# Performance work log

Hardware: AMD Instinct MI355X
Metric: run time of the kernel (lower is better)

## Reference

```python
import jax, jax.numpy as jnp
import numpy as np

E, NB, F, H = 30, 12, 1024, 32  # numEmotions, numBasicEmotions, numCommonFeatures, hidden
EPS = 1e-12  # F.normalize eps


def setup_inputs() -> dict:
    key = jax.random.key(0)
    ks = jax.random.split(key, 7)
    B, L = 8192, 128
    return {
        "basicEmotionDistributions": jax.random.uniform(ks[0], (B, NB, L), dtype=jnp.float32),
        "encodedFeatures": jax.random.normal(ks[1], (B, F), dtype=jnp.float32),
        "allBasicEmotionWeights": jax.random.normal(ks[2], (E, 1, NB, 1), dtype=jnp.float32),
        "W1": jax.random.normal(ks[3], (E, F, H), dtype=jnp.float32) / np.sqrt(F),
        "b1": jax.random.normal(ks[4], (E, H), dtype=jnp.float32) * 0.01,
        "W2": jax.random.normal(ks[5], (E, H, NB), dtype=jnp.float32) / np.sqrt(H),
        "b2": jax.random.normal(ks[6], (E, NB), dtype=jnp.float32) * 0.01,
    }


def reference(basicEmotionDistributions, encodedFeatures, allBasicEmotionWeights, W1, b1, W2, b2):
    # L1-normalize exp(weights) along basic-emotion dim: (E, NB)
    ew = jnp.exp(allBasicEmotionWeights[:, 0, :, 0])  # (E, NB)
    allW = ew / jnp.maximum(jnp.sum(jnp.abs(ew), axis=1, keepdims=True), EPS)

    # Batched per-emotion 2-layer MLP: (E, B, NB)
    h = jax.nn.selu(jnp.einsum('bf,efh->ebh', encodedFeatures, W1) + b1[:, None, :])
    mlp = jnp.einsum('ebh,ehn->ebn', h, W2) + b2[:, None, :]

    # updated weights and signed L1 normalization over NB dim
    updated = allW[:, None, :] + mlp  # (E, B, NB)
    # sign(x) * normalize(|x|, p=1) == x / max(sum|x|, eps)
    w = updated / jnp.maximum(jnp.sum(jnp.abs(updated), axis=2, keepdims=True), EPS)

    # weighted sum over basic emotions, then softmax over emotion length
    mixed = jnp.einsum('ebn,bnl->ebl', w, basicEmotionDistributions)  # (E, B, L)
    return jax.nn.softmax(mixed, axis=2)
```

## Files before the change

### kernel.cpp

```cpp
#include <hip/hip_runtime.h>

#define E_ 30
#define NB_ 12
#define F_ 1024
#define H_ 32
#define B_ 8192
#define L_ 128

typedef __attribute__((ext_vector_type(8))) _Float16 half8;
typedef __attribute__((ext_vector_type(4))) float f32x4;

#define GAS(p) ((const __attribute__((address_space(1))) void*)(p))
#define LAS(p) ((__attribute__((address_space(3))) void*)(p))

__global__ __launch_bounds__(256) void cvtA(const float* __restrict__ feat,
                                            _Float16* __restrict__ out) {
    int gid = blockIdx.x * 256 + threadIdx.x;
    int k8   = gid & 3;
    int m    = (gid >> 2) & 15;
    int frag = gid >> 6;
    int mf = frag & 7;
    int kc = (frag >> 3) & 31;
    int bt = frag >> 8;
    int b  = bt * 128 + mf * 16 + m;
    int f0 = kc * 32 + k8 * 8;
    const float4* src = (const float4*)(feat + (size_t)b * 1024 + f0);
    float4 v0 = src[0], v1 = src[1];
    half8 o;
    o[0] = (_Float16)v0.x; o[1] = (_Float16)v0.y;
    o[2] = (_Float16)v0.z; o[3] = (_Float16)v0.w;
    o[4] = (_Float16)v1.x; o[5] = (_Float16)v1.y;
    o[6] = (_Float16)v1.z; o[7] = (_Float16)v1.w;
    *(half8*)(out + ((size_t)frag * 64 + k8 * 16 + m) * 8) = o;
}

__global__ __launch_bounds__(256) void cvtW1(const float* __restrict__ W1,
                                             _Float16* __restrict__ out) {
    int gid = blockIdx.x * 256 + threadIdx.x;
    int k8   = gid & 3;
    int n    = (gid >> 2) & 15;
    int frag = gid >> 6;
    int nf = frag & 1;
    int kc = (frag >> 1) & 31;
    int e  = frag >> 6;
    int h  = nf * 16 + n;
    int f0 = kc * 32 + k8 * 8;
    const float* src = W1 + ((size_t)e * 1024 + f0) * 32 + h;
    half8 o;
#pragma unroll
    for (int j = 0; j < 8; ++j) o[j] = (_Float16)src[j * 32];
    *(half8*)(out + ((size_t)frag * 64 + k8 * 16 + n) * 8) = o;
}

__global__ __launch_bounds__(256) void gemm_mlp(
    const _Float16* __restrict__ A16, const _Float16* __restrict__ W1T,
    const float* __restrict__ b1, const float* __restrict__ W2,
    const float* __restrict__ b2, const float* __restrict__ wts,
    float* __restrict__ wbuf) {
    __shared__ __align__(16) unsigned char smem[22400];
    float* h_sh = (float*)smem;
    unsigned char* Ash = smem;
    unsigned char* Bsh = smem + 16384;
    float* w2s = (float*)(smem + 20480);
    float* cb2 = (float*)(smem + 20480 + 1536);
    float* ews = cb2 + 12;

    const int tid = threadIdx.x;
    const int e  = blockIdx.x;
    const int bt = blockIdx.y;
    const int w  = tid >> 6, l = tid & 63;
    const int q  = l >> 4, lc = l & 15;

    for (int i = tid; i < 384; i += 256) w2s[i] = W2[e * 384 + i];
    if (tid < 12) {
        cb2[tid] = b2[e * 12 + tid];
        ews[tid] = __expf(wts[e * 12 + tid]);
    }

    const _Float16* Abase = A16 + (size_t)bt * 131072;
    const _Float16* Bbase = W1T + (size_t)e * 32768;

    f32x4 zero = {0.f, 0.f, 0.f, 0.f};
    f32x4 acc[2][2];
    acc[0][0] = zero; acc[0][1] = zero; acc[1][0] = zero; acc[1][1] = zero;

    for (int it = 0; it < 16; ++it) {
        const _Float16* Ait = Abase + it * 8192;
        const _Float16* Bit = Bbase + it * 2048;
#pragma unroll
        for (int i = 0; i < 4; ++i) {
            int s = w * 4 + i;
            __builtin_amdgcn_global_load_lds(GAS(Ait + s * 512 + l * 8),
                                             LAS(Ash + s * 1024), 16, 0, 0);
        }
        __builtin_amdgcn_global_load_lds(GAS(Bit + w * 512 + l * 8),
                                         LAS(Bsh + w * 1024), 16, 0, 0);
        __syncthreads();
#pragma unroll
        for (int kc2 = 0; kc2 < 2; ++kc2) {
            half8 a0  = *(half8*)(Ash + (kc2 * 8 + 2 * w + 0) * 1024 + l * 16);
            half8 a1  = *(half8*)(Ash + (kc2 * 8 + 2 * w + 1) * 1024 + l * 16);
            half8 bv0 = *(half8*)(Bsh + (kc2 * 2 + 0) * 1024 + l * 16);
            half8 bv1 = *(half8*)(Bsh + (kc2 * 2 + 1) * 1024 + l * 16);
            acc[0][0] = __builtin_amdgcn_mfma_f32_16x16x32_f16(a0, bv0, acc[0][0], 0, 0, 0);
            acc[0][1] = __builtin_amdgcn_mfma_f32_16x16x32_f16(a0, bv1, acc[0][1], 0, 0, 0);
            acc[1][0] = __builtin_amdgcn_mfma_f32_16x16x32_f16(a1, bv0, acc[1][0], 0, 0, 0);
            acc[1][1] = __builtin_amdgcn_mfma_f32_16x16x32_f16(a1, bv1, acc[1][1], 0, 0, 0);
        }
        __syncthreads();
    }

    const float b1v0 = b1[e * 32 + lc];
    const float b1v1 = b1[e * 32 + 16 + lc];
    const float SC = 1.0507009873554805f, AL = 1.6732632423543772f;
#pragma unroll
    for (int mf = 0; mf < 2; ++mf)
#pragma unroll
        for (int nf = 0; nf < 2; ++nf)
#pragma unroll
            for (int r = 0; r < 4; ++r) {
                int m   = w * 32 + mf * 16 + q * 4 + r;
                int col = nf * 16 + lc;
                float x = acc[mf][nf][r] + (nf ? b1v1 : b1v0);
                float hv = x > 0.f ? SC * x : SC * AL * (__expf(x) - 1.f);
                h_sh[m * 33 + col] = hv;
            }
    __syncthreads();

    const int m2 = tid >> 1, sub = tid & 1;
    float u[6] = {0.f, 0.f, 0.f, 0.f, 0.f, 0.f};
    const float* hrow = h_sh + m2 * 33;
#pragma unroll 8
    for (int h = 0; h < 32; ++h) {
        float hv = hrow[h];
        const float* wr = w2s + h * 12 + sub * 6;
#pragma unroll
        for (int j = 0; j < 6; ++j) u[j] += hv * wr[j];
    }
    float sew = 0.f;
#pragma unroll
    for (int i = 0; i < 12; ++i) sew += ews[i];
    sew = fmaxf(sew, 1e-12f);
    float sabs = 0.f;
#pragma unroll
    for (int j = 0; j < 6; ++j) {
        u[j] += cb2[sub * 6 + j] + ews[sub * 6 + j] / sew;
        sabs += fabsf(u[j]);
    }
    sabs += __shfl_xor(sabs, 1);
    float inv = 1.f / fmaxf(sabs, 1e-12f);
    int b = bt * 128 + m2;
    float* dst = wbuf + (size_t)b * 360 + e * 12 + sub * 6;
#pragma unroll
    for (int j = 0; j < 6; ++j) dst[j] = u[j] * inv;
}

__global__ __launch_bounds__(256) void mix_softmax(
    const float* __restrict__ dist, const float* __restrict__ wbuf,
    float* __restrict__ out) {
    __shared__ float wsm[8 * 360];
    const int tid = threadIdx.x;
    const int b0 = blockIdx.x * 8;
    for (int i = tid; i < 2880; i += 256) wsm[i] = wbuf[(size_t)b0 * 360 + i];
    __syncthreads();
    const int m = tid >> 5, l4 = tid & 31;
    const int b = b0 + m;
    const float* dbase = dist + (size_t)b * 1536 + l4 * 4;
    f32x4 d[12];
#pragma unroll
    for (int n = 0; n < 12; ++n) d[n] = *(const f32x4*)(dbase + n * 128);
    const float* wrow = wsm + m * 360;
    for (int e = 0; e < 30; ++e) {
        const float* wr = wrow + e * 12;
        f32x4 a = {0.f, 0.f, 0.f, 0.f};
#pragma unroll
        for (int n = 0; n < 12; ++n) a += wr[n] * d[n];
        float mx = fmaxf(fmaxf(a[0], a[1]), fmaxf(a[2], a[3]));
#pragma unroll
        for (int s = 16; s >= 1; s >>= 1) mx = fmaxf(mx, __shfl_xor(mx, s));
        f32x4 ex;
        ex[0] = __expf(a[0] - mx); ex[1] = __expf(a[1] - mx);
        ex[2] = __expf(a[2] - mx); ex[3] = __expf(a[3] - mx);
        float sm = ex[0] + ex[1] + ex[2] + ex[3];
#pragma unroll
        for (int s = 16; s >= 1; s >>= 1) sm += __shfl_xor(sm, s);
        f32x4 o = ex * (1.f / sm);
        *(f32x4*)(out + ((size_t)e * 8192 + b) * 128 + l4 * 4) = o;
    }
}

extern "C" void kernel_launch(void* const* d_in, const int* in_sizes, int n_in,
                              void* d_out, int out_size, void* d_ws, size_t ws_size,
                              hipStream_t stream) {
    const float* dist = (const float*)d_in[0];
    const float* feat = (const float*)d_in[1];
    const float* wts  = (const float*)d_in[2];
    const float* W1   = (const float*)d_in[3];
    const float* b1   = (const float*)d_in[4];
    const float* W2   = (const float*)d_in[5];
    const float* b2   = (const float*)d_in[6];
    float* out = (float*)d_out;

    _Float16* A16 = (_Float16*)d_ws;
    _Float16* W1T = (_Float16*)((char*)d_ws + 16777216);
    float*   wbuf = (float*)((char*)d_ws + 16777216 + 1966080);

    cvtA<<<4096, 256, 0, stream>>>(feat, A16);
    cvtW1<<<480, 256, 0, stream>>>(W1, W1T);
    dim3 g1(30, 64);
    gemm_mlp<<<g1, 256, 0, stream>>>(A16, W1T, b1, W2, b2, wts, wbuf);
    mix_softmax<<<1024, 256, 0, stream>>>(dist, wbuf, out);
}
```

Before: 256.4 us.

## Merge conversion kernels, process two emotions per GEMM block, drop softmax max

Fuses the two fp16 conversion kernels into one launch and makes each GEMM block compute two emotions, so every A tile loaded into LDS feeds twice as many MFMAs. The intermediate weight buffer is stored emotion-major, and the mixing kernel gathers it into shared memory. The softmax max-subtraction is removed on the assumption that the mixed values stay small. That assumption holds because the weights are L1-normalised and the inputs lie in [0,1), but it drops the standard overflow safeguard.

```diff
diff --git a/kernel.cpp b/kernel.cpp
--- a/kernel.cpp
+++ b/kernel.cpp
@@ -1,11 +1,4 @@
 #include <hip/hip_runtime.h>
-
-#define E_ 30
-#define NB_ 12
-#define F_ 1024
-#define H_ 32
-#define B_ 8192
-#define L_ 128
 
 typedef __attribute__((ext_vector_type(8))) _Float16 half8;
 typedef __attribute__((ext_vector_type(4))) float f32x4;
@@ -13,43 +6,44 @@
 #define GAS(p) ((const __attribute__((address_space(1))) void*)(p))
 #define LAS(p) ((__attribute__((address_space(3))) void*)(p))
 
-__global__ __launch_bounds__(256) void cvtA(const float* __restrict__ feat,
-                                            _Float16* __restrict__ out) {
-    int gid = blockIdx.x * 256 + threadIdx.x;
-    int k8   = gid & 3;
-    int m    = (gid >> 2) & 15;
-    int frag = gid >> 6;
-    int mf = frag & 7;
-    int kc = (frag >> 3) & 31;
-    int bt = frag >> 8;
-    int b  = bt * 128 + mf * 16 + m;
-    int f0 = kc * 32 + k8 * 8;
-    const float4* src = (const float4*)(feat + (size_t)b * 1024 + f0);
-    float4 v0 = src[0], v1 = src[1];
-    half8 o;
-    o[0] = (_Float16)v0.x; o[1] = (_Float16)v0.y;
-    o[2] = (_Float16)v0.z; o[3] = (_Float16)v0.w;
-    o[4] = (_Float16)v1.x; o[5] = (_Float16)v1.y;
-    o[6] = (_Float16)v1.z; o[7] = (_Float16)v1.w;
-    *(half8*)(out + ((size_t)frag * 64 + k8 * 16 + m) * 8) = o;
-}
-
-__global__ __launch_bounds__(256) void cvtW1(const float* __restrict__ W1,
-                                             _Float16* __restrict__ out) {
-    int gid = blockIdx.x * 256 + threadIdx.x;
-    int k8   = gid & 3;
-    int n    = (gid >> 2) & 15;
-    int frag = gid >> 6;
-    int nf = frag & 1;
-    int kc = (frag >> 1) & 31;
-    int e  = frag >> 6;
-    int h  = nf * 16 + n;
-    int f0 = kc * 32 + k8 * 8;
-    const float* src = W1 + ((size_t)e * 1024 + f0) * 32 + h;
-    half8 o;
-#pragma unroll
-    for (int j = 0; j < 8; ++j) o[j] = (_Float16)src[j * 32];
-    *(half8*)(out + ((size_t)frag * 64 + k8 * 16 + n) * 8) = o;
+__global__ __launch_bounds__(256) void cvt_pre(const float* __restrict__ feat,
+                                               const float* __restrict__ W1,
+                                               _Float16* __restrict__ A16,
+                                               _Float16* __restrict__ W1T) {
+    if (blockIdx.x < 4096) {
+        int gid = blockIdx.x * 256 + threadIdx.x;
+        int k8   = gid & 3;
+        int m    = (gid >> 2) & 15;
+        int frag = gid >> 6;
+        int mf = frag & 7;
+        int kc = (frag >> 3) & 31;
+        int bt = frag >> 8;
+        int b  = bt * 128 + mf * 16 + m;
+        int f0 = kc * 32 + k8 * 8;
+        const float4* src = (const float4*)(feat + (size_t)b * 1024 + f0);
+        float4 v0 = src[0], v1 = src[1];
+        half8 o;
+        o[0] = (_Float16)v0.x; o[1] = (_Float16)v0.y;
+        o[2] = (_Float16)v0.z; o[3] = (_Float16)v0.w;
+        o[4] = (_Float16)v1.x; o[5] = (_Float16)v1.y;
+        o[6] = (_Float16)v1.z; o[7] = (_Float16)v1.w;
+        *(half8*)(A16 + ((size_t)frag * 64 + k8 * 16 + m) * 8) = o;
+    } else {
+        int gid = (blockIdx.x - 4096) * 256 + threadIdx.x;
+        int k8   = gid & 3;
+        int n    = (gid >> 2) & 15;
+        int frag = gid >> 6;
+        int nf = frag & 1;
+        int kc = (frag >> 1) & 31;
+        int e  = frag >> 6;
+        int h  = nf * 16 + n;
+        int f0 = kc * 32 + k8 * 8;
+        const float* src = W1 + ((size_t)e * 1024 + f0) * 32 + h;
+        half8 o;
+#pragma unroll
+        for (int j = 0; j < 8; ++j) o[j] = (_Float16)src[j * 32];
+        *(half8*)(W1T + ((size_t)frag * 64 + k8 * 16 + n) * 8) = o;
+    }
 }
 
 __global__ __launch_bounds__(256) void gemm_mlp(
@@ -57,102 +51,122 @@
     const float* __restrict__ b1, const float* __restrict__ W2,
     const float* __restrict__ b2, const float* __restrict__ wts,
     float* __restrict__ wbuf) {
-    __shared__ __align__(16) unsigned char smem[22400];
-    float* h_sh = (float*)smem;
+    __shared__ __align__(16) unsigned char smem[28672];
     unsigned char* Ash = smem;
     unsigned char* Bsh = smem + 16384;
-    float* w2s = (float*)(smem + 20480);
-    float* cb2 = (float*)(smem + 20480 + 1536);
-    float* ews = cb2 + 12;
+    float* w2s = (float*)(smem + 24576);
+    float* cb2 = (float*)(smem + 27648);
+    float* ews = cb2 + 24;
+    float* h_sh = (float*)smem;
 
     const int tid = threadIdx.x;
-    const int e  = blockIdx.x;
+    const int e0 = blockIdx.x * 2;
     const int bt = blockIdx.y;
     const int w  = tid >> 6, l = tid & 63;
     const int q  = l >> 4, lc = l & 15;
 
-    for (int i = tid; i < 384; i += 256) w2s[i] = W2[e * 384 + i];
-    if (tid < 12) {
-        cb2[tid] = b2[e * 12 + tid];
-        ews[tid] = __expf(wts[e * 12 + tid]);
+    for (int i = tid; i < 768; i += 256) w2s[i] = W2[e0 * 384 + i];
+    if (tid < 24) {
+        cb2[tid] = b2[e0 * 12 + tid];
+        ews[tid] = __expf(wts[e0 * 12 + tid]);
     }
 
     const _Float16* Abase = A16 + (size_t)bt * 131072;
-    const _Float16* Bbase = W1T + (size_t)e * 32768;
+    const _Float16* Bbase = W1T + (size_t)e0 * 32768;
 
     f32x4 zero = {0.f, 0.f, 0.f, 0.f};
-    f32x4 acc[2][2];
-    acc[0][0] = zero; acc[0][1] = zero; acc[1][0] = zero; acc[1][1] = zero;
+    f32x4 acc[2][4];
+#pragma unroll
+    for (int i = 0; i < 2; ++i)
+#pragma unroll
+        for (int j = 0; j < 4; ++j) acc[i][j] = zero;
 
     for (int it = 0; it < 16; ++it) {
         const _Float16* Ait = Abase + it * 8192;
-        const _Float16* Bit = Bbase + it * 2048;
 #pragma unroll
         for (int i = 0; i < 4; ++i) {
             int s = w * 4 + i;
             __builtin_amdgcn_global_load_lds(GAS(Ait + s * 512 + l * 8),
                                              LAS(Ash + s * 1024), 16, 0, 0);
         }
-        __builtin_amdgcn_global_load_lds(GAS(Bit + w * 512 + l * 8),
-                                         LAS(Bsh + w * 1024), 16, 0, 0);
+#pragma unroll
+        for (int j = 0; j < 2; ++j) {
+            int f  = w * 2 + j;
+            int be = f >> 2, kn = f & 3;
+            __builtin_amdgcn_global_load_lds(
+                GAS(Bbase + be * 32768 + it * 2048 + kn * 512 + l * 8),
+                LAS(Bsh + f * 1024), 16, 0, 0);
+        }
         __syncthreads();
 #pragma unroll
         for (int kc2 = 0; kc2 < 2; ++kc2) {
             half8 a0  = *(half8*)(Ash + (kc2 * 8 + 2 * w + 0) * 1024 + l * 16);
             half8 a1  = *(half8*)(Ash + (kc2 * 8 + 2 * w + 1) * 1024 + l * 16);
-            half8 bv0 = *(half8*)(Bsh + (kc2 * 2 + 0) * 1024 + l * 16);
-            half8 bv1 = *(half8*)(Bsh + (kc2 * 2 + 1) * 1024 + l * 16);
-            acc[0][0] = __builtin_amdgcn_mfma_f32_16x16x32_f16(a0, bv0, acc[0][0], 0, 0, 0);
-            acc[0][1] = __builtin_amdgcn_mfma_f32_16x16x32_f16(a0, bv1, acc[0][1], 0, 0, 0);
-            acc[1][0] = __builtin_amdgcn_mfma_f32_16x16x32_f16(a1, bv0, acc[1][0], 0, 0, 0);
-            acc[1][1] = __builtin_amdgcn_mfma_f32_16x16x32_f16(a1, bv1, acc[1][1], 0, 0, 0);
-        }
-        __syncthreads();
-    }
-
-    const float b1v0 = b1[e * 32 + lc];
-    const float b1v1 = b1[e * 32 + 16 + lc];
+            half8 b00 = *(half8*)(Bsh + (0 + kc2 * 2 + 0) * 1024 + l * 16);
+            half8 b01 = *(half8*)(Bsh + (0 + kc2 * 2 + 1) * 1024 + l * 16);
+            half8 b10 = *(half8*)(Bsh + (4 + kc2 * 2 + 0) * 1024 + l * 16);
+            half8 b11 = *(half8*)(Bsh + (4 + kc2 * 2 + 1) * 1024 + l * 16);
+            acc[0][0] = __builtin_amdgcn_mfma_f32_16x16x32_f16(a0, b00, acc[0][0], 0, 0, 0);
+            acc[0][1] = __builtin_amdgcn_mfma_f32_16x16x32_f16(a0, b01, acc[0][1], 0, 0, 0);
+            acc[0][2] = __builtin_amdgcn_mfma_f32_16x16x32_f16(a0, b10, acc[0][2], 0, 0, 0);
+            acc[0][3] = __builtin_amdgcn_mfma_f32_16x16x32_f16(a0, b11, acc[0][3], 0, 0, 0);
+            acc[1][0] = __builtin_amdgcn_mfma_f32_16x16x32_f16(a1, b00, acc[1][0], 0, 0, 0);
+            acc[1][1] = __builtin_amdgcn_mfma_f32_16x16x32_f16(a1, b01, acc[1][1], 0, 0, 0);
+            acc[1][2] = __builtin_amdgcn_mfma_f32_16x16x32_f16(a1, b10, acc[1][2], 0, 0, 0);
+            acc[1][3] = __builtin_amdgcn_mfma_f32_16x16x32_f16(a1, b11, acc[1][3], 0, 0, 0);
+        }
+        __syncthreads();
+    }
+
     const float SC = 1.0507009873554805f, AL = 1.6732632423543772f;
-#pragma unroll
-    for (int mf = 0; mf < 2; ++mf)
-#pragma unroll
-        for (int nf = 0; nf < 2; ++nf)
-#pragma unroll
-            for (int r = 0; r < 4; ++r) {
-                int m   = w * 32 + mf * 16 + q * 4 + r;
-                int col = nf * 16 + lc;
-                float x = acc[mf][nf][r] + (nf ? b1v1 : b1v0);
-                float hv = x > 0.f ? SC * x : SC * AL * (__expf(x) - 1.f);
-                h_sh[m * 33 + col] = hv;
-            }
-    __syncthreads();
-
     const int m2 = tid >> 1, sub = tid & 1;
-    float u[6] = {0.f, 0.f, 0.f, 0.f, 0.f, 0.f};
-    const float* hrow = h_sh + m2 * 33;
+
+#pragma unroll
+    for (int eo = 0; eo < 2; ++eo) {
+        const float b1a = b1[(e0 + eo) * 32 + lc];
+        const float b1b = b1[(e0 + eo) * 32 + 16 + lc];
+#pragma unroll
+        for (int mf = 0; mf < 2; ++mf)
+#pragma unroll
+            for (int nf = 0; nf < 2; ++nf)
+#pragma unroll
+                for (int r = 0; r < 4; ++r) {
+                    int m   = w * 32 + mf * 16 + q * 4 + r;
+                    int col = nf * 16 + lc;
+                    float x = acc[mf][eo * 2 + nf][r] + (nf ? b1b : b1a);
+                    float hv = x > 0.f ? SC * x : SC * AL * (__expf(x) - 1.f);
+                    h_sh[m * 33 + col] = hv;
+                }
+        __syncthreads();
+
+        float u[6] = {0.f, 0.f, 0.f, 0.f, 0.f, 0.f};
+        const float* hrow = h_sh + m2 * 33;
+        const float* wbase = w2s + eo * 384 + sub * 6;
 #pragma unroll 8
-    for (int h = 0; h < 32; ++h) {
-        float hv = hrow[h];
-        const float* wr = w2s + h * 12 + sub * 6;
-#pragma unroll
-        for (int j = 0; j < 6; ++j) u[j] += hv * wr[j];
-    }
-    float sew = 0.f;
-#pragma unroll
-    for (int i = 0; i < 12; ++i) sew += ews[i];
-    sew = fmaxf(sew, 1e-12f);
-    float sabs = 0.f;
-#pragma unroll
-    for (int j = 0; j < 6; ++j) {
-        u[j] += cb2[sub * 6 + j] + ews[sub * 6 + j] / sew;
-        sabs += fabsf(u[j]);
-    }
-    sabs += __shfl_xor(sabs, 1);
-    float inv = 1.f / fmaxf(sabs, 1e-12f);
-    int b = bt * 128 + m2;
-    float* dst = wbuf + (size_t)b * 360 + e * 12 + sub * 6;
-#pragma unroll
-    for (int j = 0; j < 6; ++j) dst[j] = u[j] * inv;
+        for (int h = 0; h < 32; ++h) {
+            float hv = hrow[h];
+            const float* wr = wbase + h * 12;
+#pragma unroll
+            for (int j = 0; j < 6; ++j) u[j] += hv * wr[j];
+        }
+        float sew = 0.f;
+#pragma unroll
+        for (int i = 0; i < 12; ++i) sew += ews[eo * 12 + i];
+        sew = fmaxf(sew, 1e-12f);
+        float sabs = 0.f;
+#pragma unroll
+        for (int j = 0; j < 6; ++j) {
+            u[j] += cb2[eo * 12 + sub * 6 + j] + ews[eo * 12 + sub * 6 + j] / sew;
+            sabs += fabsf(u[j]);
+        }
+        sabs += __shfl_xor(sabs, 1);
+        float inv = 1.f / fmaxf(sabs, 1e-12f);
+        int b = bt * 128 + m2;
+        float* dst = wbuf + (size_t)(e0 + eo) * 98304 + b * 12 + sub * 6;
+#pragma unroll
+        for (int j = 0; j < 6; ++j) dst[j] = u[j] * inv;
+        __syncthreads();
+    }
 }
 
 __global__ __launch_bounds__(256) void mix_softmax(
@@ -161,7 +175,10 @@
     __shared__ float wsm[8 * 360];
     const int tid = threadIdx.x;
     const int b0 = blockIdx.x * 8;
-    for (int i = tid; i < 2880; i += 256) wsm[i] = wbuf[(size_t)b0 * 360 + i];
+    for (int i = tid; i < 2880; i += 256) {
+        int e = i / 96, r = i - e * 96;
+        wsm[(r / 12) * 360 + e * 12 + (r % 12)] = wbuf[(size_t)e * 98304 + b0 * 12 + r];
+    }
     __syncthreads();
     const int m = tid >> 5, l4 = tid & 31;
     const int b = b0 + m;
@@ -175,12 +192,9 @@
         f32x4 a = {0.f, 0.f, 0.f, 0.f};
 #pragma unroll
         for (int n = 0; n < 12; ++n) a += wr[n] * d[n];
-        float mx = fmaxf(fmaxf(a[0], a[1]), fmaxf(a[2], a[3]));
-#pragma unroll
-        for (int s = 16; s >= 1; s >>= 1) mx = fmaxf(mx, __shfl_xor(mx, s));
         f32x4 ex;
-        ex[0] = __expf(a[0] - mx); ex[1] = __expf(a[1] - mx);
-        ex[2] = __expf(a[2] - mx); ex[3] = __expf(a[3] - mx);
+        ex[0] = __expf(a[0]); ex[1] = __expf(a[1]);
+        ex[2] = __expf(a[2]); ex[3] = __expf(a[3]);
         float sm = ex[0] + ex[1] + ex[2] + ex[3];
 #pragma unroll
         for (int s = 16; s >= 1; s >>= 1) sm += __shfl_xor(sm, s);
@@ -205,9 +219,8 @@
     _Float16* W1T = (_Float16*)((char*)d_ws + 16777216);
     float*   wbuf = (float*)((char*)d_ws + 16777216 + 1966080);
 
-    cvtA<<<4096, 256, 0, stream>>>(feat, A16);
-    cvtW1<<<480, 256, 0, stream>>>(W1, W1T);
-    dim3 g1(30, 64);
+    cvt_pre<<<4576, 256, 0, stream>>>(feat, W1, A16, W1T);
+    dim3 g1(15, 64);
     gemm_mlp<<<g1, 256, 0, stream>>>(A16, W1T, b1, W2, b2, wts, wbuf);
     mix_softmax<<<1024, 256, 0, stream>>>(dist, wbuf, out);
 }
```

Result: no change. 253.4 us (-1.2%).
